# Kernel tuning notes

Measured on AMD Instinct MI355X. Metric: run time of the kernel, lower is better.

The kernel has to match this reference:

```python
import jax, jax.numpy as jnp
import numpy as np

DIM = 768; HEADS = 12; N_PH = 4; EXPERTS = 8; TOPK = 2; EXPERT_DIM = 3072; MEM_HEADS = 8; EPS = 1e-5


def phm_linear(x, A, S, b):
    # PHM linear: W = sum_i kron(A[i] (n,n), S[i] (out/n, in/n)) -> (out, in); y = x @ W.T + b
    out_f = A.shape[1] * S.shape[1]
    in_f = A.shape[2] * S.shape[2]
    W = jnp.einsum('iab,icd->acbd', A, S).reshape(out_f, in_f)
    return x @ W.T + b


def layernorm(x, g, b):
    m = x.mean(-1, keepdims=True)
    v = x.var(-1, keepdims=True)
    return (x - m) / jnp.sqrt(v + EPS) * g + b


def quantum_attn(x, A_qkv, S_qkv, b_qkv, A_p, S_p, b_p, w_sup, w_ent):
    B, N, C = x.shape
    hd = C // HEADS
    qkv = phm_linear(x, A_qkv, S_qkv, b_qkv).reshape(B, N, 3, HEADS, hd)
    qkv = qkv.transpose(2, 0, 3, 1, 4)  # (3,B,H,N,hd)
    q, k, v = qkv[0], qkv[1], qkv[2]
    attn = jnp.einsum('bhnd,bhmd->bhnm', q, k) * (hd ** -0.5)
    # superposition head-mixing: sup[:,i] = sum_j w_sup[i,j] * attn[:,j]
    sup = jnp.einsum('ij,bjnm->binm', w_sup, attn)
    # entanglement: ent[:,i] = tanh(sup[:,i] + sum_j w_ent[i,j] * sup[:,j])
    ent = jnp.tanh(sup + jnp.einsum('ij,bjnm->binm', w_ent, sup))
    a = jax.nn.softmax(ent, axis=-1)
    o = jnp.einsum('bhnm,bhmd->bnhd', a, v).reshape(B, N, C)
    return phm_linear(o, A_p, S_p, b_p)


def moe(x, rA, rS, rb, domain_routing, domain_id, eA, eS, eb, ndw, ndb):
    logits = phm_linear(x, rA, rS, rb) + domain_routing[domain_id]  # (B,N,E)
    topv, topi = jax.lax.top_k(logits, TOPK)
    w = jax.nn.softmax(topv, axis=-1)  # (B,N,K)
    onehot = (topi[..., None] == jnp.arange(EXPERTS)).astype(x.dtype)  # (B,N,K,E)
    gates = jnp.einsum('bnk,bnke->bne', w, onehot)  # combined top-k gate per expert

    def expert(Ae, Se, be, We, bne):
        h = jax.nn.gelu(phm_linear(x, Ae, Se, be), approximate=False)
        return h @ We.T + bne

    outs = jax.vmap(expert)(eA, eS, eb, ndw, ndb)  # (E,B,N,C)
    return jnp.einsum('bne,ebnc->bnc', gates, outs)


def mem_mha(x, mem, iw, ib, ow, ob):
    # standard MHA: queries from x (B,N,C), keys/values from memory bank (M,C) shared across batch
    B, N, C = x.shape
    dh = C // MEM_HEADS
    q = (x @ iw[:C].T + ib[:C]).reshape(B, N, MEM_HEADS, dh)
    k = (mem @ iw[C:2 * C].T + ib[C:2 * C]).reshape(-1, MEM_HEADS, dh)
    v = (mem @ iw[2 * C:].T + ib[2 * C:]).reshape(-1, MEM_HEADS, dh)
    a = jax.nn.softmax(jnp.einsum('bnhd,mhd->bhnm', q, k) * (dh ** -0.5), axis=-1)
    o = jnp.einsum('bhnm,mhd->bnhd', a, v).reshape(B, N, C)
    return o @ ow.T + ob


def fractal(x, mems, iw, ib, ow, ob, pw, pb):
    # recursive FractalMemoryBank unrolled for depth=3:
    # level l: a_l = proc_l(MHA_l(prev, mem_l)); return prev + deeper(a_l)
    a0 = mem_mha(x, mems[0], iw[0], ib[0], ow[0], ob[0]) @ pw[0].T + pb[0]
    a1 = mem_mha(a0, mems[1], iw[1], ib[1], ow[1], ob[1]) @ pw[1].T + pb[1]
    a2 = mem_mha(a1, mems[2], iw[2], ib[2], ow[2], ob[2]) @ pw[2].T + pb[2]
    return x + (a0 + (a1 + a2))


def _fwd(x, ln1_g, ln1_b, attn_qkv_A, attn_qkv_S, attn_qkv_b, attn_proj_A, attn_proj_S, attn_proj_b,
         w_sup, w_ent, ln2_g, ln2_b, router_A, router_S, router_b, domain_routing,
         exp_A, exp_S, exp_b, exp_nd_w, exp_nd_b, mem0, mem1, mem2,
         mha_in_w, mha_in_b, mha_out_w, mha_out_b, proc_w, proc_b, ln3_g, ln3_b, domain_id):
    attended = x + quantum_attn(layernorm(x, ln1_g, ln1_b), attn_qkv_A, attn_qkv_S, attn_qkv_b,
                                attn_proj_A, attn_proj_S, attn_proj_b, w_sup, w_ent)
    moe_out = moe(layernorm(attended, ln2_g, ln2_b), router_A, router_S, router_b,
                  domain_routing, domain_id, exp_A, exp_S, exp_b, exp_nd_w, exp_nd_b)
    eo = attended + moe_out
    mo = fractal(eo, (mem0, mem1, mem2), mha_in_w, mha_in_b, mha_out_w, mha_out_b, proc_w, proc_b)
    return layernorm(mo, ln3_g, ln3_b)


def setup_inputs():
    key = jax.random.key(0)
    ks = iter(jax.random.split(key, 40))

    def rn(shape, s=0.02):
        return s * jax.random.normal(next(ks), shape, dtype=jnp.float32)

    B, N = 4, 512
    ones = jnp.ones(DIM, jnp.float32)
    zeros = jnp.zeros(DIM, jnp.float32)
    return {
        'x': rn((B, N, DIM), 1.0),
        'ln1_g': ones, 'ln1_b': zeros, 'ln2_g': ones, 'ln2_b': zeros, 'ln3_g': ones, 'ln3_b': zeros,
        'attn_qkv_A': rn((N_PH, N_PH, N_PH), 0.3),
        'attn_qkv_S': rn((N_PH, 3 * DIM // N_PH, DIM // N_PH)),
        'attn_qkv_b': jnp.zeros(3 * DIM, jnp.float32),
        'attn_proj_A': rn((N_PH, N_PH, N_PH), 0.3),
        'attn_proj_S': rn((N_PH, DIM // N_PH, DIM // N_PH)),
        'attn_proj_b': zeros,
        'w_sup': rn((HEADS, HEADS), 0.2), 'w_ent': rn((HEADS, HEADS), 0.2),
        'router_A': rn((N_PH, N_PH, N_PH), 0.3),
        'router_S': rn((N_PH, EXPERTS // N_PH, DIM // N_PH)),
        'router_b': jnp.zeros(EXPERTS, jnp.float32),
        'domain_routing': rn((6, EXPERTS), 1.0),
        'exp_A': rn((EXPERTS, N_PH, N_PH, N_PH), 0.3),
        'exp_S': rn((EXPERTS, N_PH, EXPERT_DIM // N_PH, DIM // N_PH)),
        'exp_b': jnp.zeros((EXPERTS, EXPERT_DIM), jnp.float32),
        'exp_nd_w': rn((EXPERTS, DIM, EXPERT_DIM)),
        'exp_nd_b': jnp.zeros((EXPERTS, DIM), jnp.float32),
        'mem0': rn((64, DIM), 1.0), 'mem1': rn((128, DIM), 1.0), 'mem2': rn((256, DIM), 1.0),
        'mha_in_w': rn((3, 3 * DIM, DIM)), 'mha_in_b': jnp.zeros((3, 3 * DIM), jnp.float32),
        'mha_out_w': rn((3, DIM, DIM)), 'mha_out_b': jnp.zeros((3, DIM), jnp.float32),
        'proc_w': rn((3, DIM, DIM)), 'proc_b': jnp.zeros((3, DIM), jnp.float32),
        'domain_id': 2,
    }


def reference(x, ln1_g, ln1_b, ln2_g, ln2_b, ln3_g, ln3_b, attn_qkv_A, attn_qkv_S, attn_qkv_b,
              attn_proj_A, attn_proj_S, attn_proj_b, w_sup, w_ent, router_A, router_S, router_b,
              domain_routing, exp_A, exp_S, exp_b, exp_nd_w, exp_nd_b, mem0, mem1, mem2,
              mha_in_w, mha_in_b, mha_out_w, mha_out_b, proc_w, proc_b, domain_id):
    return _fwd(x, ln1_g, ln1_b, attn_qkv_A, attn_qkv_S, attn_qkv_b, attn_proj_A, attn_proj_S,
                attn_proj_b, w_sup, w_ent, ln2_g, ln2_b, router_A, router_S, router_b,
                domain_routing, exp_A, exp_S, exp_b, exp_nd_w, exp_nd_b, mem0, mem1, mem2,
                mha_in_w, mha_in_b, mha_out_w, mha_out_b, proc_w, proc_b, ln3_g, ln3_b, domain_id)
```

## Files before the change

### kernel.cpp

```cpp
#include <hip/hip_runtime.h>
#include <math.h>

#define DIM    768
#define NTOK   2048
#define NSEQ   512
#define NBATCH 4
#define NHEADS 12
#define HD     64
#define QKVC   2304
#define MHEADS 8
#define MHD    96
#define NEXP   8
#define EDIM   3072
#define DD     (DIM*DIM)

typedef unsigned short u16;
typedef __attribute__((ext_vector_type(8))) short short8;
typedef __attribute__((ext_vector_type(4))) float f32x4;

struct L3 { long a, b, c; };
struct I3 { int a, b, c; };
struct CJ { const float4* s[6]; ushort4* d[6]; int n4[6]; };

__device__ __forceinline__ float gelu_exact(float v){
    return 0.5f * v * (1.f + erff(v * 0.70710678118654752f));
}
__device__ __forceinline__ u16 f2bf(float f){
    unsigned int u = __builtin_bit_cast(unsigned int, f);
    unsigned int r = (u + 0x7FFFu + ((u >> 16) & 1u)) >> 16;
    return (u16)r;
}
__device__ __forceinline__ float bf2f(u16 b){
    unsigned int u = ((unsigned int)b) << 16;
    return __builtin_bit_cast(float, u);
}
__device__ __forceinline__ float fast_tanh(float s){
    return 1.f - 2.f/(__expf(2.f*s) + 1.f);
}
__device__ __forceinline__ void gll16(const u16* g, u16* l){
    __builtin_amdgcn_global_load_lds((const __attribute__((address_space(1))) void*)g,
                                     (__attribute__((address_space(3))) void*)l, 16, 0, 0);
}

template<int WM,int WN,int FR,int DB>
__device__ __forceinline__ void mgemm_core(
    const u16* __restrict__ Xb, int ldx, int rowBase, int rowLim,
    const u16* __restrict__ Wb, int ldw, int colBase, int colLim, int K,
    const float* __restrict__ bias,
    const float* __restrict__ res, int ldres,
    float* __restrict__ Cf, u16* __restrict__ Cb, int ldc,
    float scale, int act)
{
    constexpr int TM = 16*FR;
    constexpr int RM = WM*TM, RN = WN*TM, NT = WM*WN*64;
    constexpr int IA = (RM*8)/NT, IB = (RN*8)/NT;
    constexpr int NB = DB ? 2 : 1;
    __shared__ u16 As[NB][RM*64];
    __shared__ u16 Bs[NB][RN*64];
    int tid = threadIdx.x;
    int lane = tid & 63, w = tid >> 6;
    int wm = (w / WN) * TM, wn = (w % WN) * TM;
    const f32x4 zf = {0.f, 0.f, 0.f, 0.f};
    f32x4 acc[FR][FR];
    #pragma unroll
    for (int i=0;i<FR;i++)
        #pragma unroll
        for (int j=0;j<FR;j++) acc[i][j] = zf;

    const bool fullA = (rowBase + RM <= rowLim);
    const bool fullB = (colBase + RN <= colLim);
    const int nt = (K + 63) >> 6;
    int lr = lane & 15, lk = lane >> 4;

    auto stage = [&](int buf, int k0){
        const bool kfull = (k0 + 64 <= K);
        if (fullA && kfull) {
            #pragma unroll
            for (int it = 0; it < IA; ++it) {
                int idx = it*NT + tid;
                int r = idx >> 3, c = idx & 7;
                gll16(&Xb[(size_t)(rowBase + r)*ldx + k0 + ((c ^ (r & 7)) << 3)], &As[buf][(size_t)idx*8]);
            }
        } else {
            #pragma unroll
            for (int it = 0; it < IA; ++it) {
                int idx = it*NT + tid;
                int r = idx >> 3, c = idx & 7;
                int gr = rowBase + r;
                uint4 v = {0u,0u,0u,0u};
                if (gr < rowLim && (k0 + c*8) < K) v = *(const uint4*)&Xb[(size_t)gr*ldx + k0 + c*8];
                *(uint4*)&As[buf][r*64 + ((c ^ (r & 7)) * 8)] = v;
            }
        }
        if (fullB && kfull) {
            #pragma unroll
            for (int it = 0; it < IB; ++it) {
                int idx = it*NT + tid;
                int r = idx >> 3, c = idx & 7;
                gll16(&Wb[(size_t)(colBase + r)*ldw + k0 + ((c ^ (r & 7)) << 3)], &Bs[buf][(size_t)idx*8]);
            }
        } else {
            #pragma unroll
            for (int it = 0; it < IB; ++it) {
                int idx = it*NT + tid;
                int r = idx >> 3, c = idx & 7;
                int gc = colBase + r;
                uint4 v = {0u,0u,0u,0u};
                if (gc < colLim && (k0 + c*8) < K) v = *(const uint4*)&Wb[(size_t)gc*ldw + k0 + c*8];
                *(uint4*)&Bs[buf][r*64 + ((c ^ (r & 7)) * 8)] = v;
            }
        }
    };
    auto compute = [&](const u16* Ac, const u16* Bc){
        #pragma unroll
        for (int ks = 0; ks < 2; ++ks) {
            short8 af[FR], bfr[FR];
            #pragma unroll
            for (int mi=0; mi<FR; mi++){
                int row = wm + mi*16 + lr;
                int cidx = (ks*4 + lk) ^ (row & 7);
                af[mi] = *(const short8*)&Ac[row*64 + cidx*8];
            }
            #pragma unroll
            for (int ni=0; ni<FR; ni++){
                int col = wn + ni*16 + lr;
                int cidx = (ks*4 + lk) ^ (col & 7);
                bfr[ni] = *(const short8*)&Bc[col*64 + cidx*8];
            }
            #pragma unroll
            for (int mi=0; mi<FR; mi++)
                #pragma unroll
                for (int ni=0; ni<FR; ni++)
                    acc[mi][ni] = __builtin_amdgcn_mfma_f32_16x16x32_bf16(af[mi], bfr[ni], acc[mi][ni], 0, 0, 0);
        }
    };

    if (DB) {
        stage(0, 0);
        __syncthreads();
        for (int t = 0; t < nt; ++t) {
            if (t + 1 < nt) stage((t+1)&1, (t+1)*64);
            compute(As[t&1], Bs[t&1]);
            __syncthreads();
        }
    } else {
        for (int t = 0; t < nt; ++t) {
            stage(0, t*64);
            __syncthreads();
            compute(As[0], Bs[0]);
            __syncthreads();
        }
    }
    int lg = lane >> 4;
    #pragma unroll
    for (int mi=0; mi<FR; mi++){
        #pragma unroll
        for (int r=0; r<4; r++){
            int row = rowBase + wm + mi*16 + lg*4 + r;
            if (row >= rowLim) continue;
            #pragma unroll
            for (int ni=0; ni<FR; ni++){
                int col = colBase + wn + ni*16 + lr;
                if (col >= colLim) continue;
                float v = acc[mi][ni][r] * scale;
                if (bias) v += bias[col];
                if (act == 1) v = gelu_exact(v);
                if (Cb) Cb[(size_t)row*ldc + col] = f2bf(v);
                if (res) v += res[(size_t)row*ldres + col];
                if (Cf) Cf[(size_t)row*ldc + col] = v;
            }
        }
    }
}

template<int WM,int WN,int FR,int DB>
__global__ __launch_bounds__(WM*WN*64) void k_mgemm(
    const u16* __restrict__ X, int ldx, int M,
    const u16* __restrict__ W, int ldw, int N, int K,
    const float* __restrict__ bias, const float* __restrict__ res, int ldres,
    float* __restrict__ Cf, u16* __restrict__ Cb, int ldc, float scale, int act)
{
    constexpr int RM = WM*16*FR, RN = WN*16*FR;
    mgemm_core<WM,WN,FR,DB>(X, ldx, blockIdx.x*RM, M, W, ldw, blockIdx.y*RN, N, K,
                            bias, res, ldres, Cf, Cb, ldc, scale, act);
}

template<int WM,int WN,int FR,int DB>
__global__ __launch_bounds__(WM*WN*64) void k_mgemm_b3(
    const u16* __restrict__ X, L3 xo, int ldx, I3 Mv,
    const u16* __restrict__ W, L3 wo, int ldw, int N, int K,
    const float* __restrict__ bias, L3 bo,
    u16* __restrict__ Cb, L3 co, int ldc, float scale, int act)
{
    constexpr int RM = WM*16*FR, RN = WN*16*FR;
    int z = blockIdx.z;
    int M    = (z==0) ? Mv.a : (z==1) ? Mv.b : Mv.c;
    long xof = (z==0) ? xo.a : (z==1) ? xo.b : xo.c;
    long wof = (z==0) ? wo.a : (z==1) ? wo.b : wo.c;
    long bof = (z==0) ? bo.a : (z==1) ? bo.b : bo.c;
    long cof = (z==0) ? co.a : (z==1) ? co.b : co.c;
    if ((int)blockIdx.x * RM >= M) return;
    mgemm_core<WM,WN,FR,DB>(X + xof, ldx, blockIdx.x*RM, M, W + wof, ldw, blockIdx.y*RN, N, K,
                            bias ? bias + bof : nullptr, nullptr, 0, nullptr, Cb + cof, ldc, scale, act);
}

template<int WM,int WN,int FR,int DB>
__global__ __launch_bounds__(WM*WN*64) void k_mgemm_expert(
    const u16* __restrict__ X, int ldx,
    const u16* __restrict__ Wb, int ldw, long wStride,
    const float* __restrict__ biasB, int biasStride,
    const int* __restrict__ prefix, const int* __restrict__ cnt,
    float* __restrict__ Cf, u16* __restrict__ Cb, int ldc, int N, int K, int act)
{
    constexpr int RM = WM*16*FR, RN = WN*16*FR;
    int e = blockIdx.z;
    int n = cnt[e];
    if ((int)blockIdx.x * RM >= n) return;
    mgemm_core<WM,WN,FR,DB>(X, ldx, prefix[e] + blockIdx.x*RM, prefix[e] + n,
                            Wb + (size_t)e*wStride, ldw, blockIdx.y*RN, N, K,
                            biasB + (size_t)e*biasStride, nullptr, 0, Cf, Cb, ldc, 1.f, act);
}

template<int WM,int WN,int FR,int DB>
__global__ __launch_bounds__(WM*WN*64) void k_mgemm_qk(const u16* __restrict__ qkv, u16* __restrict__ attn)
{
    constexpr int RM = WM*16*FR, RN = WN*16*FR;
    int z = blockIdx.z, b = z / NHEADS, h = z % NHEADS;
    const u16* X = qkv + (size_t)b*NSEQ*QKVC + h*HD;
    const u16* W = qkv + (size_t)b*NSEQ*QKVC + DIM + h*HD;
    u16* C = attn + (size_t)z*NSEQ*NSEQ;
    mgemm_core<WM,WN,FR,DB>(X, QKVC, blockIdx.x*RM, NSEQ, W, QKVC, blockIdx.y*RN, NSEQ, HD,
                            nullptr, nullptr, 0, nullptr, C, NSEQ, 0.125f, 0);
}

template<int WM,int WN,int FR,int DB>
__global__ __launch_bounds__(WM*WN*64) void k_mgemm_pv(const u16* __restrict__ P, const u16* __restrict__ Vt, u16* __restrict__ o)
{
    constexpr int RM = WM*16*FR, RN = WN*16*FR;
    int z = blockIdx.z, b = z / NHEADS, h = z % NHEADS;
    const u16* X = P + (size_t)z*NSEQ*NSEQ;
    const u16* W = Vt + ((size_t)b*DIM + h*HD)*NSEQ;
    u16* C = o + (size_t)b*NSEQ*DIM + h*HD;
    mgemm_core<WM,WN,FR,DB>(X, NSEQ, blockIdx.x*RM, NSEQ, W, NSEQ, blockIdx.y*RN, HD, NSEQ,
                            nullptr, nullptr, 0, nullptr, C, DIM, 1.f, 0);
}

template<int WM,int WN,int FR,int DB>
__global__ __launch_bounds__(WM*WN*64) void k_mgemm_mempv(const u16* __restrict__ P, const u16* __restrict__ Vt,
                                                          u16* __restrict__ O, int M)
{
    constexpr int RM = WM*16*FR, RN = WN*16*FR;
    int h = blockIdx.z;
    mgemm_core<WM,WN,FR,DB>(P + (size_t)h*NTOK*M, M, blockIdx.x*RM, NTOK, Vt + (size_t)h*MHD*M, M,
                            blockIdx.y*RN, MHD, M,
                            nullptr, nullptr, 0, nullptr, O + h*MHD, DIM, 1.f, 0);
}

__global__ __launch_bounds__(256) void k_memqk_soft(
    const u16* __restrict__ q, const u16* __restrict__ kv, int ldk,
    u16* __restrict__ P, int M, float scale)
{
    constexpr int RM = 64, RN = 256, NT = 256, K = MHD;
    __shared__ u16 As[RM*64];
    __shared__ u16 Bs[RN*64];
    __shared__ float red0[RM][4];
    __shared__ float red1[RM][4];
    int h = blockIdx.y;
    int rowBase = blockIdx.x * RM;
    const u16* Xb = q + h*MHD;
    const u16* Wb = kv + h*MHD;
    int tid = threadIdx.x, lane = tid & 63, w = tid >> 6;
    int wn = w * 64;
    int lr = lane & 15, lk = lane >> 4;
    const f32x4 zf = {0.f,0.f,0.f,0.f};
    f32x4 acc[4][4];
    #pragma unroll
    for (int i=0;i<4;i++)
        #pragma unroll
        for (int j=0;j<4;j++) acc[i][j] = zf;

    for (int k0 = 0; k0 < K; k0 += 64) {
        const bool kfull = (k0 + 64 <= K);
        if (kfull) {
            #pragma unroll
            for (int it = 0; it < 2; ++it) {
                int idx = it*NT + tid;
                int r = idx >> 3, c = idx & 7;
                gll16(&Xb[(size_t)(rowBase + r)*DIM + k0 + ((c ^ (r & 7)) << 3)], &As[(size_t)idx*8]);
            }
        } else {
            #pragma unroll
            for (int it = 0; it < 2; ++it) {
                int idx = it*NT + tid;
                int r = idx >> 3, c = idx & 7;
                uint4 v = {0u,0u,0u,0u};
                if ((k0 + c*8) < K) v = *(const uint4*)&Xb[(size_t)(rowBase + r)*DIM + k0 + c*8];
                *(uint4*)&As[r*64 + ((c ^ (r & 7)) * 8)] = v;
            }
        }
        #pragma unroll
        for (int it = 0; it < 8; ++it) {
            int idx = it*NT + tid;
            int r = idx >> 3, c = idx & 7;
            uint4 v = {0u,0u,0u,0u};
            if (r < M && (k0 + c*8) < K) v = *(const uint4*)&Wb[(size_t)r*ldk + k0 + c*8];
            *(uint4*)&Bs[r*64 + ((c ^ (r & 7)) * 8)] = v;
        }
        __syncthreads();
        #pragma unroll
        for (int ks = 0; ks < 2; ++ks) {
            short8 af[4], bfr[4];
            #pragma unroll
            for (int mi=0; mi<4; mi++){
                int row = mi*16 + lr;
                int cidx = (ks*4 + lk) ^ (row & 7);
                af[mi] = *(const short8*)&As[row*64 + cidx*8];
            }
            #pragma unroll
            for (int ni=0; ni<4; ni++){
                int col = wn + ni*16 + lr;
                int cidx = (ks*4 + lk) ^ (col & 7);
                bfr[ni] = *(const short8*)&Bs[col*64 + cidx*8];
            }
            #pragma unroll
            for (int mi=0; mi<4; mi++)
                #pragma unroll
                for (int ni=0; ni<4; ni++)
                    acc[mi][ni] = __builtin_amdgcn_mfma_f32_16x16x32_bf16(af[mi], bfr[ni], acc[mi][ni], 0, 0, 0);
        }
        __syncthreads();
    }
    int lg = lane >> 4;
    float sc[4][4][4];
    float rmax[4][4];
    #pragma unroll
    for (int mi=0; mi<4; mi++){
        #pragma unroll
        for (int r=0; r<4; r++){
            float m = -1e30f;
            #pragma unroll
            for (int ni=0; ni<4; ni++){
                int col = wn + ni*16 + lr;
                float v = (col < M) ? acc[mi][ni][r]*scale : -1e30f;
                sc[mi][r][ni] = v;
                m = fmaxf(m, v);
            }
            m = fmaxf(m, __shfl_xor(m, 1));
            m = fmaxf(m, __shfl_xor(m, 2));
            m = fmaxf(m, __shfl_xor(m, 4));
            m = fmaxf(m, __shfl_xor(m, 8));
            rmax[mi][r] = m;
        }
    }
    if (lr == 0){
        #pragma unroll
        for (int mi=0; mi<4; mi++)
            #pragma unroll
            for (int r=0; r<4; r++) red0[mi*16 + lg*4 + r][w] = rmax[mi][r];
    }
    __syncthreads();
    float gmax[4][4], rsum[4][4];
    #pragma unroll
    for (int mi=0; mi<4; mi++){
        #pragma unroll
        for (int r=0; r<4; r++){
            int row = mi*16 + lg*4 + r;
            float g = fmaxf(fmaxf(red0[row][0], red0[row][1]), fmaxf(red0[row][2], red0[row][3]));
            gmax[mi][r] = g;
            float s = 0.f;
            #pragma unroll
            for (int ni=0; ni<4; ni++){
                int col = wn + ni*16 + lr;
                if (col < M) s += __expf(sc[mi][r][ni] - g);
            }
            s += __shfl_xor(s, 1);
            s += __shfl_xor(s, 2);
            s += __shfl_xor(s, 4);
            s += __shfl_xor(s, 8);
            rsum[mi][r] = s;
        }
    }
    if (lr == 0){
        #pragma unroll
        for (int mi=0; mi<4; mi++)
            #pragma unroll
            for (int r=0; r<4; r++) red1[mi*16 + lg*4 + r][w] = rsum[mi][r];
    }
    __syncthreads();
    #pragma unroll
    for (int mi=0; mi<4; mi++){
        #pragma unroll
        for (int r=0; r<4; r++){
            int row = mi*16 + lg*4 + r;
            float tot = red1[row][0] + red1[row][1] + red1[row][2] + red1[row][3];
            float inv = 1.f / tot;
            #pragma unroll
            for (int ni=0; ni<4; ni++){
                int col = wn + ni*16 + lr;
                if (col < M)
                    P[((size_t)h*NTOK + rowBase + row)*M + col] = f2bf(__expf(sc[mi][r][ni] - gmax[mi][r]) * inv);
            }
        }
    }
}

__global__ __launch_bounds__(256) void k_transw_b(const u16* __restrict__ src, u16* __restrict__ dst)
{
    int z = blockIdx.y;
    int idx = blockIdx.x*256 + threadIdx.x;
    int r = idx / DIM, c = idx % DIM;
    dst[(size_t)z*DD + (size_t)c*DIM + r] = src[(size_t)z*DD + (size_t)r*DIM + c];
}

__global__ __launch_bounds__(256) void k_transvm_b(const u16* __restrict__ kvL, u16* __restrict__ Vtm3, I3 Mv)
{
    int z = blockIdx.y;
    int M = (z==0) ? Mv.a : (z==1) ? Mv.b : Mv.c;
    int idx = blockIdx.x*256 + threadIdx.x;
    if (idx >= DIM*M) return;
    int m = idx / DIM, d = idx % DIM;
    Vtm3[(size_t)z*DIM*256 + (size_t)d*M + m] = kvL[(size_t)z*256*2*DIM + (size_t)m*2*DIM + DIM + d];
}

__global__ __launch_bounds__(256) void k_phm(
    const float* __restrict__ A, const float* __restrict__ S, void* __restrict__ W,
    int So, int Si, int inF, long Astride, long Sstride, long Wstride, int obf)
{
    int e = blockIdx.y;
    const float* Ae = A + (size_t)e*Astride;
    const float* Se = S + (size_t)e*Sstride;
    size_t idx = (size_t)blockIdx.x*256 + threadIdx.x;
    size_t total = (size_t)(So*4) * inF;
    if (idx >= total) return;
    int in = (int)(idx % inF);
    int o  = (int)(idx / inF);
    int a = o / So, c = o % So, b = in / Si, d = in % Si;
    float w = 0.f;
    #pragma unroll
    for (int i=0;i<4;i++) w = fmaf(Ae[i*16 + a*4 + b], Se[((size_t)i*So + c)*Si + d], w);
    if (obf) ((u16*)W)[(size_t)e*Wstride + idx] = f2bf(w);
    else     ((float*)W)[(size_t)e*Wstride + idx] = w;
}

__global__ __launch_bounds__(256) void k_cvt4(const float4* __restrict__ s, ushort4* __restrict__ d, int n4)
{
    for (int i = blockIdx.x*256 + threadIdx.x; i < n4; i += gridDim.x*256){
        float4 v = s[i];
        ushort4 o; o.x = f2bf(v.x); o.y = f2bf(v.y); o.z = f2bf(v.z); o.w = f2bf(v.w);
        d[i] = o;
    }
}
__global__ __launch_bounds__(256) void k_cvt_multi(CJ J)
{
    int z = blockIdx.y;
    const float4* s = J.s[z]; ushort4* d = J.d[z]; int n4 = J.n4[z];
    for (int i = blockIdx.x*256 + threadIdx.x; i < n4; i += gridDim.x*256){
        float4 v = s[i];
        ushort4 o; o.x = f2bf(v.x); o.y = f2bf(v.y); o.z = f2bf(v.z); o.w = f2bf(v.w);
        d[i] = o;
    }
}

__global__ __launch_bounds__(256) void k_bc(const float* __restrict__ pw, const float* __restrict__ outb,
                                            const float* __restrict__ pb, float* __restrict__ bc)
{
    int l = blockIdx.y;
    int i = blockIdx.x*4 + (threadIdx.x >> 6);
    int lane = threadIdx.x & 63;
    const float* pr = pw + ((size_t)l*DIM + i)*DIM;
    const float* ob = outb + (size_t)l*DIM;
    float s = 0.f;
    for (int j = lane; j < DIM; j += 64) s = fmaf(pr[j], ob[j], s);
    for (int off=32; off; off>>=1) s += __shfl_xor(s, off);
    if (lane == 0) bc[(size_t)l*DIM + i] = s + pb[(size_t)l*DIM + i];
}

__global__ __launch_bounds__(256) void k_ln(const float* __restrict__ x, const float* __restrict__ g,
                                            const float* __restrict__ b,
                                            float* __restrict__ yf, u16* __restrict__ yb)
{
    int row = blockIdx.x, tid = threadIdx.x;
    const float* xr = x + (size_t)row * DIM;
    float v0 = xr[tid], v1 = xr[tid+256], v2 = xr[tid+512];
    float s = v0+v1+v2;
    float ss = v0*v0 + v1*v1 + v2*v2;
    for (int off=32; off; off>>=1){ s += __shfl_xor(s,off); ss += __shfl_xor(ss,off); }
    __shared__ float sa[4], sb[4];
    int wid = tid >> 6;
    if ((tid & 63) == 0){ sa[wid]=s; sb[wid]=ss; }
    __syncthreads();
    s  = sa[0]+sa[1]+sa[2]+sa[3];
    ss = sb[0]+sb[1]+sb[2]+sb[3];
    float mean = s * (1.f/DIM);
    float var  = ss * (1.f/DIM) - mean*mean;
    float rstd = rsqrtf(var + 1e-5f);
    float o0 = (v0-mean)*rstd*g[tid]     + b[tid];
    float o1 = (v1-mean)*rstd*g[tid+256] + b[tid+256];
    float o2 = (v2-mean)*rstd*g[tid+512] + b[tid+512];
    if (yf){ float* yr = yf + (size_t)row*DIM; yr[tid]=o0; yr[tid+256]=o1; yr[tid+512]=o2; }
    if (yb){ u16* yr = yb + (size_t)row*DIM; yr[tid]=f2bf(o0); yr[tid+256]=f2bf(o1); yr[tid+512]=f2bf(o2); }
}

__global__ __launch_bounds__(256) void k_supsoft(
    const u16* __restrict__ attn, u16* __restrict__ P,
    const float* __restrict__ wsup, const float* __restrict__ went)
{
    __shared__ float S[NHEADS][NSEQ];
    __shared__ float ws[144], we[144];
    int bn = blockIdx.x;
    int b = bn >> 9, n = bn & 511;
    int tid = threadIdx.x;
    if (tid < 144){ ws[tid] = wsup[tid]; we[tid] = went[tid]; }
    size_t base = ((size_t)b*NHEADS*NSEQ + n)*NSEQ;
    #pragma unroll
    for (int it=0; it<12; ++it){
        int idx = it*256 + tid;
        int j = idx >> 8, m2 = (idx & 255) * 2;
        unsigned int v = *(const unsigned int*)&attn[base + (size_t)j*NSEQ*NSEQ + m2];
        S[j][m2]   = bf2f((u16)(v & 0xFFFFu));
        S[j][m2+1] = bf2f((u16)(v >> 16));
    }
    __syncthreads();
    #pragma unroll
    for (int half=0; half<2; ++half){
        int m = tid + half*256;
        float av[12], sup[12];
        #pragma unroll
        for (int j=0;j<12;j++) av[j] = S[j][m];
        #pragma unroll
        for (int i=0;i<12;i++){
            float s = 0.f;
            #pragma unroll
            for (int j=0;j<12;j++) s = fmaf(ws[i*12+j], av[j], s);
            sup[i] = s;
        }
        #pragma unroll
        for (int i=0;i<12;i++){
            float s = sup[i];
            #pragma unroll
            for (int j=0;j<12;j++) s = fmaf(we[i*12+j], sup[j], s);
            av[i] = fast_tanh(s);
        }
        #pragma unroll
        for (int i=0;i<12;i++) S[i][m] = av[i];
    }
    __syncthreads();
    int lane = tid & 63, wv = tid >> 6;
    #pragma unroll
    for (int jj=0; jj<3; ++jj){
        int j = wv*3 + jj;
        float v[8], mx = -1e30f;
        #pragma unroll
        for (int k=0;k<8;k++){ v[k] = S[j][lane + 64*k]; mx = fmaxf(mx, v[k]); }
        for (int off=32; off; off>>=1) mx = fmaxf(mx, __shfl_xor(mx, off));
        float sum = 0.f;
        #pragma unroll
        for (int k=0;k<8;k++){ v[k] = __expf(v[k]-mx); sum += v[k]; }
        for (int off=32; off; off>>=1) sum += __shfl_xor(sum, off);
        float inv = 1.f/sum;
        #pragma unroll
        for (int k=0;k<8;k++) P[base + (size_t)j*NSEQ*NSEQ + lane + 64*k] = f2bf(v[k]*inv);
    }
}

__global__ __launch_bounds__(256) void k_transv(const u16* __restrict__ qkv, u16* __restrict__ Vt)
{
    __shared__ u16 L[64][65];
    int mt = blockIdx.x*64, dt = blockIdx.y*64, b = blockIdx.z;
    int tid = threadIdx.x;
    #pragma unroll
    for (int it=0; it<16; ++it){
        int idx = it*256 + tid;
        int mm = idx >> 6, dd = idx & 63;
        L[mm][dd] = qkv[((size_t)b*NSEQ + mt + mm)*QKVC + 1536 + dt + dd];
    }
    __syncthreads();
    #pragma unroll
    for (int it=0; it<16; ++it){
        int idx = it*256 + tid;
        int dd = idx >> 6, mm = idx & 63;
        Vt[((size_t)b*DIM + dt + dd)*NSEQ + mt + mm] = L[mm][dd];
    }
}

__global__ __launch_bounds__(256) void k_route(
    const float* __restrict__ ln2, const float* __restrict__ Wr,
    const float* __restrict__ rb, const float* __restrict__ dr,
    const int* __restrict__ did, int* __restrict__ topi, float* __restrict__ topw, int* __restrict__ cnt)
{
    int t = blockIdx.x, tid = threadIdx.x;
    const float* xr = ln2 + (size_t)t*DIM;
    float a[8] = {};
    #pragma unroll
    for (int ii=0; ii<3; ii++){
        int i = tid + ii*256;
        float xv = xr[i];
        #pragma unroll
        for (int e=0;e<8;e++) a[e] = fmaf(xv, Wr[e*DIM + i], a[e]);
    }
    #pragma unroll
    for (int e=0;e<8;e++)
        for (int off=32; off; off>>=1) a[e] += __shfl_xor(a[e], off);
    __shared__ float sred[4][8];
    int wid = tid >> 6;
    if ((tid & 63) == 0){
        #pragma unroll
        for (int e=0;e<8;e++) sred[wid][e] = a[e];
    }
    __syncthreads();
    if (tid == 0){
        int d = did[0];
        float lg[8];
        #pragma unroll
        for (int e=0;e<8;e++) lg[e] = sred[0][e]+sred[1][e]+sred[2][e]+sred[3][e] + rb[e] + dr[d*8+e];
        int i1 = 0; float v1 = lg[0];
        #pragma unroll
        for (int e=1;e<8;e++) if (lg[e] > v1){ v1 = lg[e]; i1 = e; }
        int i2 = -1; float v2 = -1e30f;
        #pragma unroll
        for (int e=0;e<8;e++) if (e != i1 && lg[e] > v2){ v2 = lg[e]; i2 = e; }
        float e2 = __expf(v2 - v1);
        float inv = 1.f / (1.f + e2);
        topi[2*t] = i1; topi[2*t+1] = i2;
        topw[2*t] = inv; topw[2*t+1] = e2 * inv;
        atomicAdd(&cnt[i1], 1); atomicAdd(&cnt[i2], 1);
    }
}

__global__ void k_zero(int* p, int n){ int i = threadIdx.x; if (i < n) p[i] = 0; }

__global__ void k_prefix(const int* __restrict__ cnt, int* __restrict__ prefix){
    if (threadIdx.x == 0){ int s=0; for (int e=0;e<8;e++){ prefix[e]=s; s+=cnt[e]; } }
}

__global__ __launch_bounds__(256) void k_assign(
    const int* __restrict__ topi, const int* __restrict__ prefix,
    int* __restrict__ cnt2, int* __restrict__ rowof, int* __restrict__ tokof)
{
    int t = blockIdx.x*256 + threadIdx.x;
    if (t >= NTOK) return;
    #pragma unroll
    for (int k=0;k<2;k++){
        int e = topi[2*t+k];
        int slot = atomicAdd(&cnt2[e], 1);
        int row = prefix[e] + slot;
        rowof[2*t+k] = row;
        tokof[row] = t;
    }
}

__global__ __launch_bounds__(256) void k_gather(const u16* __restrict__ src, const int* __restrict__ tokof, u16* __restrict__ dst)
{
    int i = blockIdx.x*256 + threadIdx.x;
    int row = i / 96, c = (i % 96) * 8;
    *(uint4*)&dst[(size_t)row*DIM + c] = *(const uint4*)&src[(size_t)tokof[row]*DIM + c];
}

__global__ __launch_bounds__(256) void k_combine(
    const float* __restrict__ att, const float* __restrict__ outg,
    const int* __restrict__ rowof, const float* __restrict__ topw,
    float* __restrict__ eo, u16* __restrict__ eob)
{
    size_t i = (size_t)blockIdx.x*256 + threadIdx.x;
    int t = (int)(i / DIM), c = (int)(i % DIM);
    int r0 = rowof[2*t], r1 = rowof[2*t+1];
    float v = att[i] + topw[2*t]*outg[(size_t)r0*DIM+c] + topw[2*t+1]*outg[(size_t)r1*DIM+c];
    eo[i] = v;
    eob[i] = f2bf(v);
}

extern "C" void kernel_launch(void* const* d_in, const int* in_sizes, int n_in,
                              void* d_out, int out_size, void* d_ws, size_t ws_size,
                              hipStream_t stream)
{
    const float* x     = (const float*)d_in[0];
    const float* ln1g  = (const float*)d_in[1];
    const float* ln1b  = (const float*)d_in[2];
    const float* ln2g  = (const float*)d_in[3];
    const float* ln2b  = (const float*)d_in[4];
    const float* ln3g  = (const float*)d_in[5];
    const float* ln3b  = (const float*)d_in[6];
    const float* qkvA  = (const float*)d_in[7];
    const float* qkvS  = (const float*)d_in[8];
    const float* qkvb  = (const float*)d_in[9];
    const float* projA = (const float*)d_in[10];
    const float* projS = (const float*)d_in[11];
    const float* projb = (const float*)d_in[12];
    const float* wsup  = (const float*)d_in[13];
    const float* went  = (const float*)d_in[14];
    const float* rA    = (const float*)d_in[15];
    const float* rS    = (const float*)d_in[16];
    const float* rb    = (const float*)d_in[17];
    const float* dr    = (const float*)d_in[18];
    const float* eA    = (const float*)d_in[19];
    const float* eS    = (const float*)d_in[20];
    const float* eb    = (const float*)d_in[21];
    const float* ndw   = (const float*)d_in[22];
    const float* ndb   = (const float*)d_in[23];
    const float* mem0  = (const float*)d_in[24];
    const float* mem1  = (const float*)d_in[25];
    const float* mem2  = (const float*)d_in[26];
    const float* inw   = (const float*)d_in[27];
    const float* inb   = (const float*)d_in[28];
    const float* outw  = (const float*)d_in[29];
    const float* outb  = (const float*)d_in[30];
    const float* pw    = (const float*)d_in[31];
    const float* pb    = (const float*)d_in[32];
    const int*   did   = (const int*)d_in[33];

    float* f = (float*)d_ws;
    size_t off = 0;
    auto alloc = [&](size_t n){ float* p = f + off; off += (n + 3) & ~(size_t)3; return p; };
    auto allocb = [&](size_t n){ return (u16*)alloc((n + 1) / 2); };

    float* lnbuf  = alloc((size_t)NTOK*DIM);
    float* attnd  = alloc((size_t)NTOK*DIM);
    float* eo     = alloc((size_t)NTOK*DIM);
    float* accum  = alloc((size_t)NTOK*DIM);
    float* attnb  = alloc((size_t)48*NSEQ*NSEQ);
    float* Wrout  = alloc((size_t)NEXP*DIM);
    float* topw   = alloc((size_t)2*NTOK);
    float* bcb    = alloc((size_t)3*DIM);
    int* ip = (int*)alloc((size_t)6*NTOK + 64);
    int* topi   = ip;            ip += 2*NTOK;
    int* rowof  = ip;            ip += 2*NTOK;
    int* tokof  = ip;            ip += 2*NTOK;
    int* cnt    = ip;            ip += 8;
    int* cnt2   = ip;            ip += 8;
    int* prefix = ip;            ip += 8;

    u16*   scores = (u16*)attnb;
    float* outg   = attnb;
    u16*   ndw_bf = (u16*)(attnb + (size_t)3146240);

    u16* Wqkv_bf  = allocb((size_t)QKVC*DIM);
    u16* Wproj_bf = allocb((size_t)DD);
    u16* Wexp_bf  = allocb((size_t)NEXP*EDIM*DIM);
    u16* inw_bf   = allocb((size_t)3*QKVC*DIM);
    u16* outw_bf  = allocb((size_t)3*DD);
    u16* pw_bf    = allocb((size_t)3*DD);
    u16* Wc_bf    = allocb((size_t)3*DD);
    u16* wT3_bf   = allocb((size_t)3*DD);
    u16* mem_bf   = allocb((size_t)448*DIM);
    u16* qkv_bf   = allocb((size_t)NTOK*QKVC);
    u16* Vt_bf    = allocb((size_t)NBATCH*DIM*NSEQ);
    u16* P_bf     = allocb((size_t)48*NSEQ*NSEQ);
    u16* lnx_bf   = allocb((size_t)NTOK*DIM);
    u16* o_bf     = allocb((size_t)NTOK*DIM);
    u16* inx_bf   = allocb((size_t)NTOK*DIM);
    u16* mhao_bf  = allocb((size_t)NTOK*DIM);
    u16* kvL_bf   = allocb((size_t)3*256*2*DIM);
    u16* Vtm3_bf  = allocb((size_t)3*DIM*256);
    u16* Xg_bf    = qkv_bf;
    u16* hidden_bf= P_bf;
    u16* Pm_bf    = P_bf;
    u16* qm_bf    = o_bf;

    float* outf = (float*)d_out;
    dim3 T256(256), T64(64);
    I3 Ms3 = {64, 128, 256};

    k_zero<<<1, 32, 0, stream>>>(cnt, 16);
    k_ln<<<NTOK, T256, 0, stream>>>(x, ln1g, ln1b, nullptr, lnx_bf);
    k_phm<<<dim3((QKVC*DIM+255)/256,1), T256, 0, stream>>>(qkvA, qkvS, Wqkv_bf, 576, 192, DIM, 0,0,0, 1);
    k_phm<<<dim3((DD+255)/256,1),  T256, 0, stream>>>(projA, projS, Wproj_bf, 192, 192, DIM, 0,0,0, 1);
    k_phm<<<dim3((NEXP*DIM+255)/256,1), T256, 0, stream>>>(rA, rS, Wrout, 2, 192, DIM, 0,0,0, 0);
    k_phm<<<dim3((EDIM*DIM+255)/256,NEXP), T256, 0, stream>>>(eA, eS, Wexp_bf, 768, 192, DIM,
                                                              64L, (long)4*768*192, (long)EDIM*DIM, 1);
    {
        CJ J;
        J.s[0]=(const float4*)inw;  J.d[0]=(ushort4*)inw_bf;  J.n4[0]=3*QKVC*DIM/4;
        J.s[1]=(const float4*)outw; J.d[1]=(ushort4*)outw_bf; J.n4[1]=3*DD/4;
        J.s[2]=(const float4*)pw;   J.d[2]=(ushort4*)pw_bf;   J.n4[2]=3*DD/4;
        J.s[3]=(const float4*)mem0; J.d[3]=(ushort4*)mem_bf;              J.n4[3]=64*DIM/4;
        J.s[4]=(const float4*)mem1; J.d[4]=(ushort4*)(mem_bf + 64*DIM);   J.n4[4]=128*DIM/4;
        J.s[5]=(const float4*)mem2; J.d[5]=(ushort4*)(mem_bf + 192*DIM);  J.n4[5]=256*DIM/4;
        k_cvt_multi<<<dim3(1024, 6), T256, 0, stream>>>(J);
    }
    k_bc<<<dim3(DIM/4, 3), T256, 0, stream>>>(pw, outb, pb, bcb);
    k_transw_b<<<dim3(DD/256, 3), T256, 0, stream>>>(outw_bf, wT3_bf);
    {
        L3 dd3 = {0, DD, 2*DD}, z3 = {0,0,0};
        I3 m768 = {DIM, DIM, DIM};
        k_mgemm_b3<2,2,2,1><<<dim3(12,12,3), T256, 0, stream>>>(pw_bf, dd3, DIM, m768,
                                                                wT3_bf, dd3, DIM, DIM, DIM,
                                                                nullptr, z3, Wc_bf, dd3, DIM, 1.f, 0);
    }
    {
        L3 xo = {0, 64L*DIM, 192L*DIM};
        L3 wo = {(long)DD, (long)QKVC*DIM + DD, 2L*QKVC*DIM + DD};
        L3 bo = {(long)DIM, (long)QKVC + DIM, 2L*QKVC + DIM};
        L3 co = {0, 256L*2*DIM, 2*256L*2*DIM};
        k_mgemm_b3<1,1,2,1><<<dim3(8,48,3), T64, 0, stream>>>(mem_bf, xo, DIM, Ms3,
                                                              inw_bf, wo, DIM, 2*DIM, DIM,
                                                              inb, bo, kvL_bf, co, 2*DIM, 1.f, 0);
    }
    k_transvm_b<<<dim3((DIM*256)/256, 3), T256, 0, stream>>>(kvL_bf, Vtm3_bf, Ms3);

    k_mgemm<2,2,4,0><<<dim3(16,18), T256, 0, stream>>>(lnx_bf, DIM, NTOK, Wqkv_bf, DIM, QKVC, DIM,
                                                       qkvb, nullptr, 0, nullptr, qkv_bf, QKVC, 1.f, 0);
    k_transv<<<dim3(8,12,NBATCH), T256, 0, stream>>>(qkv_bf, Vt_bf);
    k_mgemm_qk<2,2,4,0><<<dim3(4,4,48), T256, 0, stream>>>(qkv_bf, scores);
    k_supsoft<<<dim3(NTOK), T256, 0, stream>>>(scores, P_bf, wsup, went);
    k_cvt4<<<4096, T256, 0, stream>>>((const float4*)ndw, (ushort4*)ndw_bf, NEXP*DIM*EDIM/4);
    k_mgemm_pv<1,1,2,1><<<dim3(16,2,48), T64, 0, stream>>>(P_bf, Vt_bf, o_bf);
    k_mgemm<2,2,2,1><<<dim3(32,12), T256, 0, stream>>>(o_bf, DIM, NTOK, Wproj_bf, DIM, DIM, DIM,
                                                       projb, x, DIM, attnd, nullptr, DIM, 1.f, 0);
    k_ln<<<NTOK, T256, 0, stream>>>(attnd, ln2g, ln2b, lnbuf, lnx_bf);
    k_route<<<NTOK, T256, 0, stream>>>(lnbuf, Wrout, rb, dr, did, topi, topw, cnt);
    k_prefix<<<1, 1, 0, stream>>>(cnt, prefix);
    k_assign<<<8, T256, 0, stream>>>(topi, prefix, cnt2, rowof, tokof);
    k_gather<<<dim3(1536), T256, 0, stream>>>(lnx_bf, tokof, Xg_bf);
    k_mgemm_expert<2,2,4,0><<<dim3(16,24,NEXP), T256, 0, stream>>>(Xg_bf, DIM, Wexp_bf, DIM, (long)EDIM*DIM,
                                                                   eb, EDIM, prefix, cnt,
                                                                   nullptr, hidden_bf, EDIM, EDIM, DIM, 1);
    k_mgemm_expert<2,2,2,1><<<dim3(32,12,NEXP), T256, 0, stream>>>(hidden_bf, EDIM, ndw_bf, EDIM, (long)DIM*EDIM,
                                                                   ndb, DIM, prefix, cnt,
                                                                   outg, nullptr, DIM, DIM, EDIM, 0);
    k_combine<<<dim3(6144), T256, 0, stream>>>(attnd, outg, rowof, topw, eo, inx_bf);
    int Ms[3] = {64, 128, 256};
    for (int l=0; l<3; ++l){
        const u16* iwl = inw_bf + (size_t)l*QKVC*DIM;
        int M = Ms[l];
        k_mgemm<2,2,2,1><<<dim3(32,12), T256, 0, stream>>>(inx_bf, DIM, NTOK, iwl, DIM, DIM, DIM,
                                                           inb + (size_t)l*QKVC, nullptr, 0, nullptr, qm_bf, DIM, 1.f, 0);
        k_memqk_soft<<<dim3(NTOK/64, MHEADS), T256, 0, stream>>>(qm_bf, kvL_bf + (size_t)l*256*2*DIM, 2*DIM,
                                                                 Pm_bf, M, 0.10206207261596577f);
        k_mgemm_mempv<1,1,2,1><<<dim3(64,3,MHEADS), T64, 0, stream>>>(Pm_bf, Vtm3_bf + (size_t)l*DIM*256, mhao_bf, M);
        k_mgemm<2,2,2,1><<<dim3(32,12), T256, 0, stream>>>(mhao_bf, DIM, NTOK, Wc_bf + (size_t)l*DD, DIM, DIM, DIM,
                                                           bcb + (size_t)l*DIM, (l==0 ? eo : accum), DIM,
                                                           accum, inx_bf, DIM, 1.f, 0);
    }
    k_ln<<<NTOK, T256, 0, stream>>>(accum, ln3g, ln3b, outf, nullptr);
}
```

Before: 686.0 us.

## Pipeline GEMM tile loads with vmcnt waits and shrink big-GEMM tiles

Rewrites the double-buffered GEMM main loop. When tiles are full and K is a multiple of 64, the next tile's global-to-LDS loads are issued first, then a partial s_waitcnt vmcnt waits only for the current tile before a raw s_barrier, so loads overlap compute. The QKV, QK and first expert GEMMs switch from single-buffered 128x128 tiles to double-buffered 64x64 tiles with four times as many blocks. This aims to hide memory latency and improve occupancy, at the cost of less data reuse per tile and reliance on hand-counted vmcnt values being correct.

```diff
diff --git a/kernel.cpp b/kernel.cpp
--- a/kernel.cpp
+++ b/kernel.cpp
@@ -41,6 +41,11 @@
     __builtin_amdgcn_global_load_lds((const __attribute__((address_space(1))) void*)g,
                                      (__attribute__((address_space(3))) void*)l, 16, 0, 0);
 }
+__device__ __forceinline__ void pipe_barrier(){
+    asm volatile("" ::: "memory");
+    __builtin_amdgcn_s_barrier();
+    asm volatile("" ::: "memory");
+}
 
 template<int WM,int WN,int FR,int DB>
 __device__ __forceinline__ void mgemm_core(
@@ -54,9 +59,9 @@
     constexpr int TM = 16*FR;
     constexpr int RM = WM*TM, RN = WN*TM, NT = WM*WN*64;
     constexpr int IA = (RM*8)/NT, IB = (RN*8)/NT;
-    constexpr int NB = DB ? 2 : 1;
-    __shared__ u16 As[NB][RM*64];
-    __shared__ u16 Bs[NB][RN*64];
+    constexpr int NLD = IA + IB;
+    __shared__ u16 As[2][RM*64];
+    __shared__ u16 Bs[2][RN*64];
     int tid = threadIdx.x;
     int lane = tid & 63, w = tid >> 6;
     int wm = (w / WN) * TM, wn = (w % WN) * TM;
@@ -72,43 +77,38 @@
     const int nt = (K + 63) >> 6;
     int lr = lane & 15, lk = lane >> 4;
 
-    auto stage = [&](int buf, int k0){
-        const bool kfull = (k0 + 64 <= K);
-        if (fullA && kfull) {
-            #pragma unroll
-            for (int it = 0; it < IA; ++it) {
-                int idx = it*NT + tid;
-                int r = idx >> 3, c = idx & 7;
-                gll16(&Xb[(size_t)(rowBase + r)*ldx + k0 + ((c ^ (r & 7)) << 3)], &As[buf][(size_t)idx*8]);
-            }
-        } else {
-            #pragma unroll
-            for (int it = 0; it < IA; ++it) {
-                int idx = it*NT + tid;
-                int r = idx >> 3, c = idx & 7;
-                int gr = rowBase + r;
-                uint4 v = {0u,0u,0u,0u};
-                if (gr < rowLim && (k0 + c*8) < K) v = *(const uint4*)&Xb[(size_t)gr*ldx + k0 + c*8];
-                *(uint4*)&As[buf][r*64 + ((c ^ (r & 7)) * 8)] = v;
-            }
-        }
-        if (fullB && kfull) {
-            #pragma unroll
-            for (int it = 0; it < IB; ++it) {
-                int idx = it*NT + tid;
-                int r = idx >> 3, c = idx & 7;
-                gll16(&Wb[(size_t)(colBase + r)*ldw + k0 + ((c ^ (r & 7)) << 3)], &Bs[buf][(size_t)idx*8]);
-            }
-        } else {
-            #pragma unroll
-            for (int it = 0; it < IB; ++it) {
-                int idx = it*NT + tid;
-                int r = idx >> 3, c = idx & 7;
-                int gc = colBase + r;
-                uint4 v = {0u,0u,0u,0u};
-                if (gc < colLim && (k0 + c*8) < K) v = *(const uint4*)&Wb[(size_t)gc*ldw + k0 + c*8];
-                *(uint4*)&Bs[buf][r*64 + ((c ^ (r & 7)) * 8)] = v;
-            }
+    auto stage_fast = [&](int buf, int k0){
+        #pragma unroll
+        for (int it = 0; it < IA; ++it) {
+            int idx = it*NT + tid;
+            int r = idx >> 3, c = idx & 7;
+            gll16(&Xb[(size_t)(rowBase + r)*ldx + k0 + ((c ^ (r & 7)) << 3)], &As[buf][(size_t)idx*8]);
+        }
+        #pragma unroll
+        for (int it = 0; it < IB; ++it) {
+            int idx = it*NT + tid;
+            int r = idx >> 3, c = idx & 7;
+            gll16(&Wb[(size_t)(colBase + r)*ldw + k0 + ((c ^ (r & 7)) << 3)], &Bs[buf][(size_t)idx*8]);
+        }
+    };
+    auto stage_guard = [&](int buf, int k0){
+        #pragma unroll
+        for (int it = 0; it < IA; ++it) {
+            int idx = it*NT + tid;
+            int r = idx >> 3, c = idx & 7;
+            int gr = rowBase + r;
+            uint4 v = {0u,0u,0u,0u};
+            if (gr < rowLim && (k0 + c*8) < K) v = *(const uint4*)&Xb[(size_t)gr*ldx + k0 + c*8];
+            *(uint4*)&As[buf][r*64 + ((c ^ (r & 7)) * 8)] = v;
+        }
+        #pragma unroll
+        for (int it = 0; it < IB; ++it) {
+            int idx = it*NT + tid;
+            int r = idx >> 3, c = idx & 7;
+            int gc = colBase + r;
+            uint4 v = {0u,0u,0u,0u};
+            if (gc < colLim && (k0 + c*8) < K) v = *(const uint4*)&Wb[(size_t)gc*ldw + k0 + c*8];
+            *(uint4*)&Bs[buf][r*64 + ((c ^ (r & 7)) * 8)] = v;
         }
     };
     auto compute = [&](const u16* Ac, const u16* Bc){
@@ -135,17 +135,26 @@
         }
     };
 
-    if (DB) {
-        stage(0, 0);
-        __syncthreads();
+    const bool pipe = DB && fullA && fullB && ((K & 63) == 0);
+    if (pipe) {
+        stage_fast(0, 0);
         for (int t = 0; t < nt; ++t) {
-            if (t + 1 < nt) stage((t+1)&1, (t+1)*64);
+            if (t + 1 < nt) {
+                stage_fast((t+1)&1, (t+1)*64);
+                if constexpr (NLD == 4)      asm volatile("s_waitcnt vmcnt(4)" ::: "memory");
+                else if constexpr (NLD == 8) asm volatile("s_waitcnt vmcnt(8)" ::: "memory");
+                else                         asm volatile("s_waitcnt vmcnt(0)" ::: "memory");
+            } else {
+                asm volatile("s_waitcnt vmcnt(0)" ::: "memory");
+            }
+            __builtin_amdgcn_s_barrier();
+            asm volatile("" ::: "memory");
             compute(As[t&1], Bs[t&1]);
-            __syncthreads();
+            pipe_barrier();
         }
     } else {
         for (int t = 0; t < nt; ++t) {
-            stage(0, t*64);
+            stage_guard(0, t*64);
             __syncthreads();
             compute(As[0], Bs[0]);
             __syncthreads();
@@ -797,10 +806,10 @@
     }
     k_transvm_b<<<dim3((DIM*256)/256, 3), T256, 0, stream>>>(kvL_bf, Vtm3_bf, Ms3);
 
-    k_mgemm<2,2,4,0><<<dim3(16,18), T256, 0, stream>>>(lnx_bf, DIM, NTOK, Wqkv_bf, DIM, QKVC, DIM,
+    k_mgemm<2,2,2,1><<<dim3(32,36), T256, 0, stream>>>(lnx_bf, DIM, NTOK, Wqkv_bf, DIM, QKVC, DIM,
                                                        qkvb, nullptr, 0, nullptr, qkv_bf, QKVC, 1.f, 0);
     k_transv<<<dim3(8,12,NBATCH), T256, 0, stream>>>(qkv_bf, Vt_bf);
-    k_mgemm_qk<2,2,4,0><<<dim3(4,4,48), T256, 0, stream>>>(qkv_bf, scores);
+    k_mgemm_qk<2,2,2,1><<<dim3(8,8,48), T256, 0, stream>>>(qkv_bf, scores);
     k_supsoft<<<dim3(NTOK), T256, 0, stream>>>(scores, P_bf, wsup, went);
     k_cvt4<<<4096, T256, 0, stream>>>((const float4*)ndw, (ushort4*)ndw_bf, NEXP*DIM*EDIM/4);
     k_mgemm_pv<1,1,2,1><<<dim3(16,2,48), T64, 0, stream>>>(P_bf, Vt_bf, o_bf);
@@ -811,7 +820,7 @@
     k_prefix<<<1, 1, 0, stream>>>(cnt, prefix);
     k_assign<<<8, T256, 0, stream>>>(topi, prefix, cnt2, rowof, tokof);
     k_gather<<<dim3(1536), T256, 0, stream>>>(lnx_bf, tokof, Xg_bf);
-    k_mgemm_expert<2,2,4,0><<<dim3(16,24,NEXP), T256, 0, stream>>>(Xg_bf, DIM, Wexp_bf, DIM, (long)EDIM*DIM,
+    k_mgemm_expert<2,2,2,1><<<dim3(32,48,NEXP), T256, 0, stream>>>(Xg_bf, DIM, Wexp_bf, DIM, (long)EDIM*DIM,
                                                                    eb, EDIM, prefix, cnt,
                                                                    nullptr, hidden_bf, EDIM, EDIM, DIM, 1);
     k_mgemm_expert<2,2,2,1><<<dim3(32,12,NEXP), T256, 0, stream>>>(hidden_bf, EDIM, ndw_bf, EDIM, (long)DIM*EDIM,
```

After: 717.7 us. +4.6%, slower.

## Fold memory-MHA value projection into combined output weight and retune GEMM tiles

Applied to the files above, without the earlier changes.

Precomputes Gt = Wc_head · V_memᵀ per layer and head, so each memory-attention layer becomes a single GEMM of the head-interleaved softmax probabilities (K = 8·M) against Gt. This replaces the separate P·V GEMM, the V transpose kernel and the extra output projection pass. The softmax kernel now writes P in a token-major, head-interleaved layout to suit this. It also changes tile configurations for the QKV, QK^T and expert down-projection GEMMs, which alters grid sizes and double-buffering choices.

```diff
diff --git a/kernel.cpp b/kernel.cpp
--- a/kernel.cpp
+++ b/kernel.cpp
@@ -246,14 +246,18 @@
 }
 
 template<int WM,int WN,int FR,int DB>
-__global__ __launch_bounds__(WM*WN*64) void k_mgemm_mempv(const u16* __restrict__ P, const u16* __restrict__ Vt,
-                                                          u16* __restrict__ O, int M)
+__global__ __launch_bounds__(WM*WN*64) void k_gt(
+    const u16* __restrict__ Wc, const u16* __restrict__ kvL, long kvStride,
+    u16* __restrict__ Gt, long gtStride, I3 Mv)
 {
     constexpr int RM = WM*16*FR, RN = WN*16*FR;
-    int h = blockIdx.z;
-    mgemm_core<WM,WN,FR,DB>(P + (size_t)h*NTOK*M, M, blockIdx.x*RM, NTOK, Vt + (size_t)h*MHD*M, M,
-                            blockIdx.y*RN, MHD, M,
-                            nullptr, nullptr, 0, nullptr, O + h*MHD, DIM, 1.f, 0);
+    int z = blockIdx.z, l = z >> 3, h = z & 7;
+    int M = (l==0) ? Mv.a : (l==1) ? Mv.b : Mv.c;
+    if ((int)blockIdx.y * RN >= M) return;
+    mgemm_core<WM,WN,FR,DB>(Wc + (size_t)l*DD + h*MHD, DIM, blockIdx.x*RM, DIM,
+                            kvL + (size_t)l*kvStride + DIM + h*MHD, 2*DIM, blockIdx.y*RN, M, MHD,
+                            nullptr, nullptr, 0, nullptr,
+                            Gt + (size_t)l*gtStride + (size_t)h*M, 8*M, 1.f, 0);
 }
 
 __global__ __launch_bounds__(256) void k_memqk_soft(
@@ -398,7 +402,7 @@
             for (int ni=0; ni<4; ni++){
                 int col = wn + ni*16 + lr;
                 if (col < M)
-                    P[((size_t)h*NTOK + rowBase + row)*M + col] = f2bf(__expf(sc[mi][r][ni] - gmax[mi][r]) * inv);
+                    P[(((size_t)(rowBase + row))*MHEADS + h)*M + col] = f2bf(__expf(sc[mi][r][ni] - gmax[mi][r]) * inv);
             }
         }
     }
@@ -410,16 +414,6 @@
     int idx = blockIdx.x*256 + threadIdx.x;
     int r = idx / DIM, c = idx % DIM;
     dst[(size_t)z*DD + (size_t)c*DIM + r] = src[(size_t)z*DD + (size_t)r*DIM + c];
-}
-
-__global__ __launch_bounds__(256) void k_transvm_b(const u16* __restrict__ kvL, u16* __restrict__ Vtm3, I3 Mv)
-{
-    int z = blockIdx.y;
-    int M = (z==0) ? Mv.a : (z==1) ? Mv.b : Mv.c;
-    int idx = blockIdx.x*256 + threadIdx.x;
-    if (idx >= DIM*M) return;
-    int m = idx / DIM, d = idx % DIM;
-    Vtm3[(size_t)z*DIM*256 + (size_t)d*M + m] = kvL[(size_t)z*256*2*DIM + (size_t)m*2*DIM + DIM + d];
 }
 
 __global__ __launch_bounds__(256) void k_phm(
@@ -748,9 +742,8 @@
     u16* lnx_bf   = allocb((size_t)NTOK*DIM);
     u16* o_bf     = allocb((size_t)NTOK*DIM);
     u16* inx_bf   = allocb((size_t)NTOK*DIM);
-    u16* mhao_bf  = allocb((size_t)NTOK*DIM);
     u16* kvL_bf   = allocb((size_t)3*256*2*DIM);
-    u16* Vtm3_bf  = allocb((size_t)3*DIM*256);
+    u16* Gt_bf    = allocb((size_t)3*768*2048);
     u16* Xg_bf    = qkv_bf;
     u16* hidden_bf= P_bf;
     u16* Pm_bf    = P_bf;
@@ -795,12 +788,12 @@
                                                               inw_bf, wo, DIM, 2*DIM, DIM,
                                                               inb, bo, kvL_bf, co, 2*DIM, 1.f, 0);
     }
-    k_transvm_b<<<dim3((DIM*256)/256, 3), T256, 0, stream>>>(kvL_bf, Vtm3_bf, Ms3);
-
-    k_mgemm<2,2,4,0><<<dim3(16,18), T256, 0, stream>>>(lnx_bf, DIM, NTOK, Wqkv_bf, DIM, QKVC, DIM,
+    k_gt<2,2,2,1><<<dim3(12,4,24), T256, 0, stream>>>(Wc_bf, kvL_bf, 256L*2*DIM, Gt_bf, 768L*2048, Ms3);
+
+    k_mgemm<2,2,2,1><<<dim3(32,36), T256, 0, stream>>>(lnx_bf, DIM, NTOK, Wqkv_bf, DIM, QKVC, DIM,
                                                        qkvb, nullptr, 0, nullptr, qkv_bf, QKVC, 1.f, 0);
     k_transv<<<dim3(8,12,NBATCH), T256, 0, stream>>>(qkv_bf, Vt_bf);
-    k_mgemm_qk<2,2,4,0><<<dim3(4,4,48), T256, 0, stream>>>(qkv_bf, scores);
+    k_mgemm_qk<2,2,2,1><<<dim3(8,8,48), T256, 0, stream>>>(qkv_bf, scores);
     k_supsoft<<<dim3(NTOK), T256, 0, stream>>>(scores, P_bf, wsup, went);
     k_cvt4<<<4096, T256, 0, stream>>>((const float4*)ndw, (ushort4*)ndw_bf, NEXP*DIM*EDIM/4);
     k_mgemm_pv<1,1,2,1><<<dim3(16,2,48), T64, 0, stream>>>(P_bf, Vt_bf, o_bf);
@@ -814,9 +807,9 @@
     k_mgemm_expert<2,2,4,0><<<dim3(16,24,NEXP), T256, 0, stream>>>(Xg_bf, DIM, Wexp_bf, DIM, (long)EDIM*DIM,
                                                                    eb, EDIM, prefix, cnt,
                                                                    nullptr, hidden_bf, EDIM, EDIM, DIM, 1);
-    k_mgemm_expert<2,2,2,1><<<dim3(32,12,NEXP), T256, 0, stream>>>(hidden_bf, EDIM, ndw_bf, EDIM, (long)DIM*EDIM,
-                                                                   ndb, DIM, prefix, cnt,
-                                                                   outg, nullptr, DIM, DIM, EDIM, 0);
+    k_mgemm_expert<2,2,4,0><<<dim3(16,6,NEXP), T256, 0, stream>>>(hidden_bf, EDIM, ndw_bf, EDIM, (long)DIM*EDIM,
+                                                                  ndb, DIM, prefix, cnt,
+                                                                  outg, nullptr, DIM, DIM, EDIM, 0);
     k_combine<<<dim3(6144), T256, 0, stream>>>(attnd, outg, rowof, topw, eo, inx_bf);
     int Ms[3] = {64, 128, 256};
     for (int l=0; l<3; ++l){
@@ -826,8 +819,7 @@
                                                            inb + (size_t)l*QKVC, nullptr, 0, nullptr, qm_bf, DIM, 1.f, 0);
         k_memqk_soft<<<dim3(NTOK/64, MHEADS), T256, 0, stream>>>(qm_bf, kvL_bf + (size_t)l*256*2*DIM, 2*DIM,
                                                                  Pm_bf, M, 0.10206207261596577f);
-        k_mgemm_mempv<1,1,2,1><<<dim3(64,3,MHEADS), T64, 0, stream>>>(Pm_bf, Vtm3_bf + (size_t)l*DIM*256, mhao_bf, M);
-        k_mgemm<2,2,2,1><<<dim3(32,12), T256, 0, stream>>>(mhao_bf, DIM, NTOK, Wc_bf + (size_t)l*DD, DIM, DIM, DIM,
+        k_mgemm<2,2,2,1><<<dim3(32,12), T256, 0, stream>>>(Pm_bf, 8*M, NTOK, Gt_bf + (size_t)l*768*2048, 8*M, DIM, 8*M,
                                                            bcb + (size_t)l*DIM, (l==0 ? eo : accum), DIM,
                                                            accum, inx_bf, DIM, 1.f, 0);
     }
```

After: 713.8 us. 4.1% more time.
